# Kernel optimization log

Hardware: AMD Instinct MI355X
Metric: run time of the kernel (lower is better)

Reference implementation:

```python
import jax, jax.numpy as jnp
import numpy as np

N, E = 50000, 800000
IN_CH, EDGE_DIM, H, C = 256, 32, 4, 32


def setup_inputs() -> dict:
    key = jax.random.key(0)
    ks = jax.random.split(key, 9)
    inp = {
        "x": jax.random.normal(ks[0], (N, IN_CH), dtype=jnp.float32),
        "edge_index": jax.random.randint(ks[1], (2, E), 0, N, dtype=jnp.int64),
        "edge_attr": jax.random.normal(ks[2], (E, EDGE_DIM), dtype=jnp.float32),
        "dist_weight": jax.random.uniform(ks[3], (E,), dtype=jnp.float32),
        # learned parameters (xavier-ish scale)
        "W_src": jax.random.normal(ks[4], (IN_CH, H * C), dtype=jnp.float32) * (1.0 / np.sqrt(IN_CH)),
        "W_dst": jax.random.normal(ks[5], (IN_CH, H * C), dtype=jnp.float32) * (1.0 / np.sqrt(IN_CH)),
        "W_edge": jax.random.normal(ks[6], (EDGE_DIM, H * C), dtype=jnp.float32) * (1.0 / np.sqrt(EDGE_DIM)),
        "att": jax.random.normal(ks[7], (1, H, C), dtype=jnp.float32) * 0.1,
        "spatial_scale": jnp.ones((H,), dtype=jnp.float32),
    }
    return inp


def reference(x, edge_index, edge_attr, dist_weight, W_src, W_dst, W_edge, att, spatial_scale):
    n = x.shape[0]
    h, c = att.shape[1], att.shape[2]
    src, dst = edge_index[0], edge_index[1]

    x_src = (x @ W_src).reshape(n, h, c)          # [N,H,C]
    x_dst = (x @ W_dst).reshape(n, h, c)          # [N,H,C]
    e_feat = (edge_attr @ W_edge).reshape(-1, h, c)  # [E,H,C]

    # edge-wise attention logits
    alpha = jnp.tanh(x_src[src] + x_dst[dst] + e_feat)  # [E,H,C]
    alpha = jnp.sum(alpha * att, axis=-1)               # [E,H]
    alpha_raw = alpha

    # spatial decay: dist_weight ** spatial_scale per head
    alpha = alpha * dist_weight[:, None] ** spatial_scale[None, :]

    # segment softmax over dst (numerically stable; max is grad-neutral)
    m = jax.ops.segment_max(alpha, dst, num_segments=n)  # [N,H]
    m = jnp.where(jnp.isfinite(m), m, 0.0)               # empty segments -> 0 (matches torch init)
    m = jax.lax.stop_gradient(m)
    ea = jnp.exp(alpha - m[dst])                         # [E,H]
    s = jax.ops.segment_sum(ea, dst, num_segments=n)     # [N,H]
    alpha_norm = ea / (s[dst] + 1e-8)                    # [E,H]

    # weighted aggregation of source features
    msg = x_src[src] * alpha_norm[:, :, None]            # [E,H,C]
    out = jax.ops.segment_sum(msg, dst, num_segments=n)  # [N,H,C]
    return out.reshape(n, h * c), alpha_norm, alpha_raw
```

## Files before the change

### kernel.cpp

```cpp
#include <hip/hip_runtime.h>
#include <hip/hip_bf16.h>

#define N_NODES 50000
#define N_EDGES 800000
#define IN_CH   256
#define EDGE_DIM 32
#define NH 4
#define NC 32
#define HC 128
#define SCAN_BLKS 196
#define EGROUPS (N_EDGES / 64)
#define NTILES (N_NODES / 16)

typedef __attribute__((ext_vector_type(8))) short bf16x8;
typedef __attribute__((ext_vector_type(4))) float f32x4;

__device__ int g_bsum[256];
__device__ int g_boffs[256];
__device__ __align__(16) unsigned short g_wt_hi[256 * 256];
__device__ __align__(16) unsigned short g_wt_lo[256 * 256];

__device__ __forceinline__ float fexp2(float x) { return __builtin_amdgcn_exp2f(x); }
__device__ __forceinline__ float flog2(float x) { return __builtin_amdgcn_logf(x); }
__device__ __forceinline__ float fexp(float x)  { return __builtin_amdgcn_exp2f(x * 1.44269504089f); }

__device__ __forceinline__ float ftanh(float x) {
    const float e = fexp2(x * 2.88539008178f);
    return 1.0f - 2.0f * __builtin_amdgcn_rcpf(e + 1.0f);
}

__device__ __forceinline__ unsigned short f2bf(float f) {
    union { float f; unsigned int u; } v; v.f = f;
    const unsigned int r = v.u + 0x7fffu + ((v.u >> 16) & 1u);
    return (unsigned short)(r >> 16);
}

__device__ __forceinline__ void split8(const float4 a, const float4 b, bf16x8& hi, bf16x8& lo) {
    union { unsigned short us[8]; bf16x8 v; } H, L;
    const float xs[8] = {a.x, a.y, a.z, a.w, b.x, b.y, b.z, b.w};
    #pragma unroll
    for (int e = 0; e < 8; ++e) {
        const unsigned int u = __float_as_uint(xs[e]);
        H.us[e] = (unsigned short)(u >> 16);
        const float lof = xs[e] - __uint_as_float(u & 0xffff0000u);
        L.us[e] = (unsigned short)(__float_as_uint(lof) >> 16);
    }
    hi = H.v; lo = L.v;
}

__device__ __forceinline__ float ldf(const void* p, long i, bool f32) {
    return f32 ? ((const float*)p)[i]
               : __bfloat162float(((const __hip_bfloat16*)p)[i]);
}

__device__ __forceinline__ int ld_src(const int* ei, long e, bool idx64) {
    return idx64 ? ei[2 * e] : ei[e];
}
__device__ __forceinline__ int ld_dst(const int* ei, long e, bool idx64) {
    return idx64 ? ei[2 * ((long)N_EDGES + e)] : ei[(long)N_EDGES + e];
}

__global__ __launch_bounds__(256) void detect_k(const unsigned short* __restrict__ xu,
                                                const int* __restrict__ ei,
                                                int* __restrict__ flag) {
    __shared__ int zc, bc, nz_idx;
    if (threadIdx.x == 0) { zc = 0; bc = 0; nz_idx = 0; }
    __syncthreads();
    int z = 0, b = 0, hi = 0;
    for (int i = threadIdx.x; i < 16384; i += 256) {
        const unsigned short w = xu[2 * i];
        if (w == 0) ++z;
        if ((w & 0x7F80) == 0x7F80) ++b;
    }
    for (int i = threadIdx.x; i < 8192; i += 256)
        if (ei[2 * i + 1] != 0) hi = 1;
    atomicAdd(&zc, z);
    atomicAdd(&bc, b);
    if (hi) atomicAdd(&nz_idx, 1);
    __syncthreads();
    if (threadIdx.x == 0) {
        flag[0] = (zc > 8192 || bc > 0) ? 1 : 0;
        flag[1] = (nz_idx == 0) ? 1 : 0;
    }
}

__global__ __launch_bounds__(256) void zero_deg_k(int* __restrict__ deg) {
    const int i = blockIdx.x * 256 + threadIdx.x;
    if (i < N_NODES) deg[i] = 0;
}

__global__ __launch_bounds__(256) void hist_k(const int* __restrict__ ei,
                                              const int* __restrict__ flag,
                                              int* __restrict__ deg) {
    const bool idx64 = (flag[1] != 0);
    const long e = (long)blockIdx.x * 256 + threadIdx.x;
    if (e < N_EDGES) atomicAdd(&deg[ld_dst(ei, e, idx64)], 1);
}

__global__ __launch_bounds__(256) void scan1_k(const int* __restrict__ deg,
                                               int* __restrict__ row_ptr) {
    __shared__ int wsum[4];
    const int tid = threadIdx.x;
    const int lane = tid & 63, wid = tid >> 6;
    const int i = blockIdx.x * 256 + tid;
    const int v = (i < N_NODES) ? deg[i] : 0;
    int x = v;
    #pragma unroll
    for (int off = 1; off < 64; off <<= 1) {
        const int t = __shfl_up(x, off);
        if (lane >= off) x += t;
    }
    if (lane == 63) wsum[wid] = x;
    __syncthreads();
    int wpre = 0;
    for (int w = 0; w < wid; ++w) wpre += wsum[w];
    if (i < N_NODES) row_ptr[i] = wpre + x - v;
    if (tid == 0) g_bsum[blockIdx.x] = wsum[0] + wsum[1] + wsum[2] + wsum[3];
}

__global__ __launch_bounds__(256) void scan2_k(int* __restrict__ row_ptr) {
    __shared__ int wsum[4];
    const int tid = threadIdx.x;
    const int lane = tid & 63, wid = tid >> 6;
    const int v = (tid < SCAN_BLKS) ? g_bsum[tid] : 0;
    int x = v;
    #pragma unroll
    for (int off = 1; off < 64; off <<= 1) {
        const int t = __shfl_up(x, off);
        if (lane >= off) x += t;
    }
    if (lane == 63) wsum[wid] = x;
    __syncthreads();
    int wpre = 0;
    for (int w = 0; w < wid; ++w) wpre += wsum[w];
    if (tid < SCAN_BLKS) g_boffs[tid] = wpre + x - v;
    if (tid == 0) row_ptr[N_NODES] = N_EDGES;
}

__global__ __launch_bounds__(256) void scan3_k(int* __restrict__ row_ptr,
                                               int* __restrict__ cursor) {
    const int i = blockIdx.x * 256 + threadIdx.x;
    if (i < N_NODES) {
        const int t = row_ptr[i] + g_boffs[blockIdx.x];
        row_ptr[i] = t;
        cursor[i] = t;
    }
}

__global__ __launch_bounds__(256) void scatter_k(const int* __restrict__ ei,
                                                 const int* __restrict__ flag,
                                                 int* __restrict__ cursor,
                                                 int* __restrict__ eids,
                                                 int* __restrict__ esrc) {
    const bool idx64 = (flag[1] != 0);
    const long e = (long)blockIdx.x * 256 + threadIdx.x;
    if (e >= N_EDGES) return;
    const int dst = ld_dst(ei, e, idx64);
    const int src = ld_src(ei, e, idx64);
    const int pos = atomicAdd(&cursor[dst], 1);
    eids[pos] = (int)e;
    esrc[pos] = src;
}

__global__ __launch_bounds__(256) void w_split_k(const float* __restrict__ Wsrc,
                                                 const float* __restrict__ Wdst,
                                                 const int* __restrict__ flag) {
    if (flag[0] == 0) return;
    const int i = blockIdx.x * 256 + threadIdx.x;
    const int c = i >> 8;
    const int k = i & 255;
    const float w = (c < HC) ? Wsrc[k * HC + c] : Wdst[k * HC + (c - HC)];
    const unsigned int u = __float_as_uint(w);
    g_wt_hi[i] = (unsigned short)(u >> 16);
    const float lof = w - __uint_as_float(u & 0xffff0000u);
    g_wt_lo[i] = (unsigned short)(__float_as_uint(lof) >> 16);
}

__global__ __launch_bounds__(512) void node_gemm_f32s_k(const float* __restrict__ x,
                                                        const int* __restrict__ flag,
                                                        float* __restrict__ xsrc,
                                                        float* __restrict__ xdst) {
    if (flag[0] == 0) return;
    const int tid = threadIdx.x;
    const int l   = tid & 63;
    const int wv  = tid >> 6;
    const int jj  = l & 15;
    const int hi4 = l >> 4;
    const int cbase = wv * 32;

    bf16x8 bhi[8][2], blo[8][2];
    #pragma unroll
    for (int ks = 0; ks < 8; ++ks)
        #pragma unroll
        for (int t = 0; t < 2; ++t) {
            const int off = (cbase + t * 16 + jj) * 256 + ks * 32 + hi4 * 8;
            bhi[ks][t] = *(const bf16x8*)(g_wt_hi + off);
            blo[ks][t] = *(const bf16x8*)(g_wt_lo + off);
        }

    for (int nt = blockIdx.x; nt < NTILES; nt += gridDim.x) {
        const long n0 = (long)nt * 16;
        const float* xr = x + (n0 + jj) * IN_CH;

        f32x4 acc[2];
        acc[0] = (f32x4){0.f, 0.f, 0.f, 0.f};
        acc[1] = (f32x4){0.f, 0.f, 0.f, 0.f};
        #pragma unroll
        for (int ks = 0; ks < 8; ++ks) {
            const float4 a0 = *(const float4*)(xr + ks * 32 + hi4 * 8);
            const float4 a1 = *(const float4*)(xr + ks * 32 + hi4 * 8 + 4);
            bf16x8 ahi, alo;
            split8(a0, a1, ahi, alo);
            #pragma unroll
            for (int t = 0; t < 2; ++t) {
                acc[t] = __builtin_amdgcn_mfma_f32_16x16x32_bf16(ahi, bhi[ks][t], acc[t], 0, 0, 0);
                acc[t] = __builtin_amdgcn_mfma_f32_16x16x32_bf16(ahi, blo[ks][t], acc[t], 0, 0, 0);
                acc[t] = __builtin_amdgcn_mfma_f32_16x16x32_bf16(alo, bhi[ks][t], acc[t], 0, 0, 0);
            }
        }

        #pragma unroll
        for (int t = 0; t < 2; ++t) {
            const int c = cbase + t * 16 + jj;
            float* obase = (c < HC) ? (xsrc + c) : (xdst + (c - HC));
            #pragma unroll
            for (int r = 0; r < 4; ++r)
                obase[(n0 + hi4 * 4 + r) * HC] = acc[t][r];
        }
    }
}

__global__ __launch_bounds__(256) void node_gemm_mfma_k(const unsigned short* __restrict__ x,
                                                        const unsigned short* __restrict__ Wsrc,
                                                        const unsigned short* __restrict__ Wdst,
                                                        const int* __restrict__ flag,
                                                        float* __restrict__ xsrc,
                                                        float* __restrict__ xdst) {
    if (flag[0] != 0) return;
    const int tid = threadIdx.x;
    const int l   = tid & 63;
    const int w   = tid >> 6;
    const int jj  = l & 15;
    const int hi  = l >> 4;
    const int cbase = w * 64;

    bf16x8 bfrag[8][4];
    #pragma unroll
    for (int ks = 0; ks < 8; ++ks)
        #pragma unroll
        for (int t = 0; t < 4; ++t) {
            const int c = cbase + t * 16 + jj;
            const unsigned short* Wp = (c < HC) ? (Wsrc + c) : (Wdst + (c - HC));
            union { unsigned short u[8]; bf16x8 v; } bu;
            #pragma unroll
            for (int i = 0; i < 8; ++i)
                bu.u[i] = Wp[(ks * 32 + hi * 8 + i) * HC];
            bfrag[ks][t] = bu.v;
        }

    for (int nt = blockIdx.x; nt < NTILES; nt += gridDim.x) {
        const long n0 = (long)nt * 16;
        const unsigned short* xr = x + (n0 + jj) * IN_CH + hi * 8;
        bf16x8 afrag[8];
        #pragma unroll
        for (int ks = 0; ks < 8; ++ks)
            afrag[ks] = *(const bf16x8*)(xr + ks * 32);

        f32x4 acc[4];
        #pragma unroll
        for (int t = 0; t < 4; ++t) acc[t] = (f32x4){0.f, 0.f, 0.f, 0.f};
        #pragma unroll
        for (int ks = 0; ks < 8; ++ks)
            #pragma unroll
            for (int t = 0; t < 4; ++t)
                acc[t] = __builtin_amdgcn_mfma_f32_16x16x32_bf16(afrag[ks], bfrag[ks][t], acc[t], 0, 0, 0);

        #pragma unroll
        for (int t = 0; t < 4; ++t) {
            const int c = cbase + t * 16 + jj;
            float* obase = (c < HC) ? (xsrc + c) : (xdst + (c - HC));
            #pragma unroll
            for (int r = 0; r < 4; ++r)
                obase[(n0 + hi * 4 + r) * HC] = acc[t][r];
        }
    }
}

__global__ __launch_bounds__(256) void edge_alpha_k(const int* __restrict__ ei,
                                                    const void* __restrict__ eattr,
                                                    const void* __restrict__ dw,
                                                    const void* __restrict__ Wedge,
                                                    const void* __restrict__ att,
                                                    const void* __restrict__ sscale,
                                                    const int* __restrict__ flag,
                                                    const float* __restrict__ xsrc,
                                                    const float* __restrict__ xdst,
                                                    float* __restrict__ ea_ws,
                                                    float* __restrict__ araw_out) {
    const bool f32   = (flag[0] != 0);
    const bool idx64 = (flag[1] != 0);
    __shared__ int   sSrc[4][16];
    __shared__ int   sDst[4][16];
    __shared__ float sDw[4][16];

    const int tid = threadIdx.x;
    const int l   = tid & 63;
    const int wid = tid >> 6;
    const int jj  = l & 15;
    const int hi  = l >> 4;

    bf16x8 bfrag[8];
    #pragma unroll
    for (int t = 0; t < 8; ++t) {
        union { unsigned short u[8]; bf16x8 v; } bu;
        #pragma unroll
        for (int i = 0; i < 8; ++i) {
            const int k = hi * 8 + i;
            const int col = t * 16 + jj;
            if (f32) bu.u[i] = f2bf(((const float*)Wedge)[k * HC + col]);
            else     bu.u[i] = ((const unsigned short*)Wedge)[k * HC + col];
        }
        bfrag[t] = bu.v;
    }
    float attv[8];
    #pragma unroll
    for (int t = 0; t < 8; ++t) attv[t] = ldf(att, t * 16 + jj, f32);
    const float ssv = ldf(sscale, l & 3, f32);

    for (long g = blockIdx.x; g < EGROUPS; g += (long)gridDim.x) {
        const long e0 = g * 64 + (long)wid * 16;

        if (l < 16)      sSrc[wid][l]      = ld_src(ei, e0 + l, idx64);
        else if (l < 32) sDst[wid][l - 16] = ld_dst(ei, e0 + (l - 16), idx64);
        else if (l < 48) sDw[wid][l - 32]  = ldf(dw, e0 + (l - 32), f32);
        __builtin_amdgcn_wave_barrier();

        bf16x8 afrag;
        if (f32) {
            const float* ar = (const float*)eattr + (e0 + jj) * EDGE_DIM + hi * 8;
            const float4 p0 = *(const float4*)ar;
            const float4 p1 = *(const float4*)(ar + 4);
            union { unsigned short u[8]; bf16x8 v; } au;
            au.u[0] = f2bf(p0.x); au.u[1] = f2bf(p0.y); au.u[2] = f2bf(p0.z); au.u[3] = f2bf(p0.w);
            au.u[4] = f2bf(p1.x); au.u[5] = f2bf(p1.y); au.u[6] = f2bf(p1.z); au.u[7] = f2bf(p1.w);
            afrag = au.v;
        } else {
            afrag = *(const bf16x8*)((const unsigned short*)eattr + (e0 + jj) * EDGE_DIM + hi * 8);
        }

        const f32x4 zero = {0.f, 0.f, 0.f, 0.f};
        f32x4 acc[8];
        #pragma unroll
        for (int t = 0; t < 8; ++t)
            acc[t] = __builtin_amdgcn_mfma_f32_16x16x32_bf16(afrag, bfrag[t], zero, 0, 0, 0);

        float hsum[4][4] = {{0,0,0,0},{0,0,0,0},{0,0,0,0},{0,0,0,0}};
        #pragma unroll
        for (int r = 0; r < 4; ++r) {
            const int sI = sSrc[wid][hi * 4 + r];
            const int dI = sDst[wid][hi * 4 + r];
            const float* bs = xsrc + (long)sI * HC + jj;
            const float* bd = xdst + (long)dI * HC + jj;
            float xsv[8], xdv[8];
            #pragma unroll
            for (int t = 0; t < 8; ++t) xsv[t] = bs[t * 16];
            #pragma unroll
            for (int t = 0; t < 8; ++t) xdv[t] = bd[t * 16];
            #pragma unroll
            for (int t = 0; t < 8; ++t) {
                const float v = ftanh(acc[t][r] + xsv[t] + xdv[t]) * attv[t];
                hsum[r][t >> 1] += v;
            }
        }

        #pragma unroll
        for (int r = 0; r < 4; ++r)
            #pragma unroll
            for (int h2 = 0; h2 < 4; ++h2) {
                float v = hsum[r][h2];
                v += __shfl_xor(v, 1);
                v += __shfl_xor(v, 2);
                v += __shfl_xor(v, 4);
                v += __shfl_xor(v, 8);
                hsum[r][h2] = v;
            }

        float val = hsum[0][0];
        #pragma unroll
        for (int r = 0; r < 4; ++r)
            #pragma unroll
            for (int h2 = 0; h2 < 4; ++h2)
                if (jj == r * 4 + h2) val = hsum[r][h2];

        const int r_sel = jj >> 2;
        const long er = e0 + hi * 4 + r_sel;
        const float dwv = sDw[wid][hi * 4 + r_sel];
        araw_out[er * 4 + (jj & 3)] = val;
        const float d = fexp2(ssv * flog2(dwv));
        ea_ws[er * 4 + (jj & 3)] = fexp(val * d);
        __builtin_amdgcn_wave_barrier();
    }
}

__global__ __launch_bounds__(256) void aggregate_k(const int* __restrict__ row_ptr,
                                                   const int* __restrict__ eids,
                                                   const int* __restrict__ esrc,
                                                   const float* __restrict__ ea_ws,
                                                   const float* __restrict__ xsrc,
                                                   float* __restrict__ s_ws,
                                                   float* __restrict__ out) {
    const int tid = threadIdx.x;
    const int lane = tid & 63;
    const int n = blockIdx.x * 4 + (tid >> 6);
    if (n >= N_NODES) return;
    const int h = lane >> 4;

    const int p0 = row_ptr[n];
    const int p1 = row_ptr[n + 1];

    float ax = 0.0f, ay = 0.0f, sa = 0.0f;
    for (int p = p0; p < p1; ++p) {
        const int e = eids[p];
        const int src = esrc[p];
        const float w = ea_ws[(long)e * 4 + h];
        const float2 xv = *(const float2*)(xsrc + (long)src * HC + (lane << 1));
        ax += w * xv.x;
        ay += w * xv.y;
        sa += w;
    }
    const float inv = 1.0f / (sa + 1e-8f);
    float* o = out + (long)n * HC + (lane << 1);
    o[0] = ax * inv;
    o[1] = ay * inv;
    if ((lane & 15) == 0) s_ws[(long)n * 4 + h] = sa;
}

__global__ __launch_bounds__(256) void edge_norm_k(const int* __restrict__ ei,
                                                   const int* __restrict__ flag,
                                                   const float* __restrict__ ea_ws,
                                                   const float* __restrict__ s_ws,
                                                   float* __restrict__ anorm) {
    const bool idx64 = (flag[1] != 0);
    const long i = (long)blockIdx.x * 256 + threadIdx.x;
    if (i >= (long)N_EDGES * NH) return;
    const long e = i >> 2;
    const int h = (int)(i & 3);
    const int dst = ld_dst(ei, e, idx64);
    anorm[i] = ea_ws[i] / (s_ws[(long)dst * 4 + h] + 1e-8f);
}

extern "C" void kernel_launch(void* const* d_in, const int* in_sizes, int n_in,
                              void* d_out, int out_size, void* d_ws, size_t ws_size,
                              hipStream_t stream) {
    const void* x      = d_in[0];
    const int*  ei     = (const int*)d_in[1];
    const void* eattr  = d_in[2];
    const void* dw     = d_in[3];
    const void* Wsrc   = d_in[4];
    const void* Wdst   = d_in[5];
    const void* Wedge  = d_in[6];
    const void* att    = d_in[7];
    const void* sscale = d_in[8];

    float* out   = (float*)d_out;
    float* anorm = out + (long)N_NODES * HC;
    float* araw  = anorm + (long)N_EDGES * NH;

    float* ws      = (float*)d_ws;
    int*   flag    = (int*)d_ws;
    float* xsrc    = ws + 64;
    float* xdst    = xsrc + (long)N_NODES * HC;
    float* ea      = xdst + (long)N_NODES * HC;
    float* s_ws    = ea + (long)N_EDGES * NH;
    int*   deg     = (int*)(s_ws + (long)N_NODES * NH);
    int*   row_ptr = deg + N_NODES;
    int*   cursor  = row_ptr + N_NODES + 1;
    int*   eids    = cursor + N_NODES;
    int*   esrc    = eids + N_EDGES;

    detect_k<<<1, 256, 0, stream>>>((const unsigned short*)x, ei, flag);
    zero_deg_k<<<(N_NODES + 255) / 256, 256, 0, stream>>>(deg);
    hist_k<<<(N_EDGES + 255) / 256, 256, 0, stream>>>(ei, flag, deg);
    scan1_k<<<SCAN_BLKS, 256, 0, stream>>>(deg, row_ptr);
    scan2_k<<<1, 256, 0, stream>>>(row_ptr);
    scan3_k<<<SCAN_BLKS, 256, 0, stream>>>(row_ptr, cursor);
    scatter_k<<<(N_EDGES + 255) / 256, 256, 0, stream>>>(ei, flag, cursor, eids, esrc);
    w_split_k<<<256, 256, 0, stream>>>((const float*)Wsrc, (const float*)Wdst, flag);
    node_gemm_f32s_k<<<512, 512, 0, stream>>>((const float*)x, flag, xsrc, xdst);
    node_gemm_mfma_k<<<1024, 256, 0, stream>>>((const unsigned short*)x,
                                               (const unsigned short*)Wsrc,
                                               (const unsigned short*)Wdst,
                                               flag, xsrc, xdst);
    edge_alpha_k<<<2048, 256, 0, stream>>>(ei, eattr, dw, Wedge, att, sscale,
                                           flag, xsrc, xdst, ea, araw);
    aggregate_k<<<(N_NODES + 3) / 4, 256, 0, stream>>>(row_ptr, eids, esrc, ea, xsrc, s_ws, out);
    edge_norm_k<<<((long)N_EDGES * NH + 255) / 256, 256, 0, stream>>>(ei, flag, ea, s_ws, anorm);
}
```

Before: 671.1 us.

## Fuse edge attention and aggregation into one destination-sorted CSR kernel

Replaces the edge-parallel attention kernel and the separate node aggregation kernel with one kernel where each wave walks a destination node's CSR edge list in chunks of 16. It computes the attention logits with MFMA, exponentiates them, and accumulates the weighted x_src messages in registers, so x_src rows are fetched once for both uses and ea_ws is no longer reread during aggregation. x_dst is loaded once per node. The costs are gathered (non-coalesced) edge_attr and dist_weight reads through the edge-id permutation, and idle lanes on nodes with fewer than 16 edges. The type-detection kernel also samples fewer elements, which makes the heuristic slightly less robust.

```diff
diff --git a/kernel.cpp b/kernel.cpp
--- a/kernel.cpp
+++ b/kernel.cpp
@@ -9,7 +9,6 @@
 #define NC 32
 #define HC 128
 #define SCAN_BLKS 196
-#define EGROUPS (N_EDGES / 64)
 #define NTILES (N_NODES / 16)
 
 typedef __attribute__((ext_vector_type(8))) short bf16x8;
@@ -67,19 +66,19 @@
     if (threadIdx.x == 0) { zc = 0; bc = 0; nz_idx = 0; }
     __syncthreads();
     int z = 0, b = 0, hi = 0;
-    for (int i = threadIdx.x; i < 16384; i += 256) {
+    for (int i = threadIdx.x; i < 4096; i += 256) {
         const unsigned short w = xu[2 * i];
         if (w == 0) ++z;
         if ((w & 0x7F80) == 0x7F80) ++b;
     }
-    for (int i = threadIdx.x; i < 8192; i += 256)
+    for (int i = threadIdx.x; i < 2048; i += 256)
         if (ei[2 * i + 1] != 0) hi = 1;
     atomicAdd(&zc, z);
     atomicAdd(&bc, b);
     if (hi) atomicAdd(&nz_idx, 1);
     __syncthreads();
     if (threadIdx.x == 0) {
-        flag[0] = (zc > 8192 || bc > 0) ? 1 : 0;
+        flag[0] = (zc > 2048 || bc > 0) ? 1 : 0;
         flag[1] = (nz_idx == 0) ? 1 : 0;
     }
 }
@@ -286,21 +285,24 @@
     }
 }
 
-__global__ __launch_bounds__(256) void edge_alpha_k(const int* __restrict__ ei,
-                                                    const void* __restrict__ eattr,
-                                                    const void* __restrict__ dw,
-                                                    const void* __restrict__ Wedge,
-                                                    const void* __restrict__ att,
-                                                    const void* __restrict__ sscale,
-                                                    const int* __restrict__ flag,
-                                                    const float* __restrict__ xsrc,
-                                                    const float* __restrict__ xdst,
-                                                    float* __restrict__ ea_ws,
-                                                    float* __restrict__ araw_out) {
-    const bool f32   = (flag[0] != 0);
-    const bool idx64 = (flag[1] != 0);
+__global__ __launch_bounds__(256) void fused_edge_agg_k(const int* __restrict__ row_ptr,
+                                                        const int* __restrict__ eids,
+                                                        const int* __restrict__ esrc,
+                                                        const void* __restrict__ eattr,
+                                                        const void* __restrict__ dw,
+                                                        const void* __restrict__ Wedge,
+                                                        const void* __restrict__ att,
+                                                        const void* __restrict__ sscale,
+                                                        const int* __restrict__ flag,
+                                                        const float* __restrict__ xsrc,
+                                                        const float* __restrict__ xdst,
+                                                        float* __restrict__ ea_ws,
+                                                        float* __restrict__ araw_out,
+                                                        float* __restrict__ s_ws,
+                                                        float* __restrict__ out) {
+    const bool f32 = (flag[0] != 0);
+    __shared__ int   sEid[4][16];
     __shared__ int   sSrc[4][16];
-    __shared__ int   sDst[4][16];
     __shared__ float sDw[4][16];
 
     const int tid = threadIdx.x;
@@ -325,114 +327,138 @@
     float attv[8];
     #pragma unroll
     for (int t = 0; t < 8; ++t) attv[t] = ldf(att, t * 16 + jj, f32);
-    const float ssv = ldf(sscale, l & 3, f32);
-
-    for (long g = blockIdx.x; g < EGROUPS; g += (long)gridDim.x) {
-        const long e0 = g * 64 + (long)wid * 16;
-
-        if (l < 16)      sSrc[wid][l]      = ld_src(ei, e0 + l, idx64);
-        else if (l < 32) sDst[wid][l - 16] = ld_dst(ei, e0 + (l - 16), idx64);
-        else if (l < 48) sDw[wid][l - 32]  = ldf(dw, e0 + (l - 32), f32);
-        __builtin_amdgcn_wave_barrier();
-
-        bf16x8 afrag;
-        if (f32) {
-            const float* ar = (const float*)eattr + (e0 + jj) * EDGE_DIM + hi * 8;
-            const float4 p0 = *(const float4*)ar;
-            const float4 p1 = *(const float4*)(ar + 4);
-            union { unsigned short u[8]; bf16x8 v; } au;
-            au.u[0] = f2bf(p0.x); au.u[1] = f2bf(p0.y); au.u[2] = f2bf(p0.z); au.u[3] = f2bf(p0.w);
-            au.u[4] = f2bf(p1.x); au.u[5] = f2bf(p1.y); au.u[6] = f2bf(p1.z); au.u[7] = f2bf(p1.w);
-            afrag = au.v;
-        } else {
-            afrag = *(const bf16x8*)((const unsigned short*)eattr + (e0 + jj) * EDGE_DIM + hi * 8);
-        }
-
-        const f32x4 zero = {0.f, 0.f, 0.f, 0.f};
-        f32x4 acc[8];
-        #pragma unroll
-        for (int t = 0; t < 8; ++t)
-            acc[t] = __builtin_amdgcn_mfma_f32_16x16x32_bf16(afrag, bfrag[t], zero, 0, 0, 0);
-
-        float hsum[4][4] = {{0,0,0,0},{0,0,0,0},{0,0,0,0},{0,0,0,0}};
-        #pragma unroll
-        for (int r = 0; r < 4; ++r) {
-            const int sI = sSrc[wid][hi * 4 + r];
-            const int dI = sDst[wid][hi * 4 + r];
-            const float* bs = xsrc + (long)sI * HC + jj;
-            const float* bd = xdst + (long)dI * HC + jj;
-            float xsv[8], xdv[8];
-            #pragma unroll
-            for (int t = 0; t < 8; ++t) xsv[t] = bs[t * 16];
-            #pragma unroll
-            for (int t = 0; t < 8; ++t) xdv[t] = bd[t * 16];
-            #pragma unroll
-            for (int t = 0; t < 8; ++t) {
-                const float v = ftanh(acc[t][r] + xsv[t] + xdv[t]) * attv[t];
-                hsum[r][t >> 1] += v;
-            }
-        }
-
-        #pragma unroll
-        for (int r = 0; r < 4; ++r)
-            #pragma unroll
-            for (int h2 = 0; h2 < 4; ++h2) {
-                float v = hsum[r][h2];
-                v += __shfl_xor(v, 1);
-                v += __shfl_xor(v, 2);
-                v += __shfl_xor(v, 4);
-                v += __shfl_xor(v, 8);
-                hsum[r][h2] = v;
-            }
-
-        float val = hsum[0][0];
-        #pragma unroll
-        for (int r = 0; r < 4; ++r)
-            #pragma unroll
-            for (int h2 = 0; h2 < 4; ++h2)
-                if (jj == r * 4 + h2) val = hsum[r][h2];
-
-        const int r_sel = jj >> 2;
-        const long er = e0 + hi * 4 + r_sel;
-        const float dwv = sDw[wid][hi * 4 + r_sel];
-        araw_out[er * 4 + (jj & 3)] = val;
-        const float d = fexp2(ssv * flog2(dwv));
-        ea_ws[er * 4 + (jj & 3)] = fexp(val * d);
-        __builtin_amdgcn_wave_barrier();
-    }
-}
-
-__global__ __launch_bounds__(256) void aggregate_k(const int* __restrict__ row_ptr,
-                                                   const int* __restrict__ eids,
-                                                   const int* __restrict__ esrc,
-                                                   const float* __restrict__ ea_ws,
-                                                   const float* __restrict__ xsrc,
-                                                   float* __restrict__ s_ws,
-                                                   float* __restrict__ out) {
-    const int tid = threadIdx.x;
-    const int lane = tid & 63;
-    const int n = blockIdx.x * 4 + (tid >> 6);
-    if (n >= N_NODES) return;
-    const int h = lane >> 4;
-
-    const int p0 = row_ptr[n];
-    const int p1 = row_ptr[n + 1];
-
-    float ax = 0.0f, ay = 0.0f, sa = 0.0f;
-    for (int p = p0; p < p1; ++p) {
-        const int e = eids[p];
-        const int src = esrc[p];
-        const float w = ea_ws[(long)e * 4 + h];
-        const float2 xv = *(const float2*)(xsrc + (long)src * HC + (lane << 1));
-        ax += w * xv.x;
-        ay += w * xv.y;
-        sa += w;
-    }
-    const float inv = 1.0f / (sa + 1e-8f);
-    float* o = out + (long)n * HC + (lane << 1);
-    o[0] = ax * inv;
-    o[1] = ay * inv;
-    if ((lane & 15) == 0) s_ws[(long)n * 4 + h] = sa;
+    float ss4[4];
+    #pragma unroll
+    for (int h2 = 0; h2 < 4; ++h2) ss4[h2] = ldf(sscale, h2, f32);
+
+    const int nwaves = gridDim.x * 4;
+    for (int n = blockIdx.x * 4 + wid; n < N_NODES; n += nwaves) {
+        const int p0 = row_ptr[n];
+        const int p1 = row_ptr[n + 1];
+
+        float xdv[8];
+        #pragma unroll
+        for (int t = 0; t < 8; ++t) xdv[t] = xdst[(long)n * HC + jj + t * 16];
+
+        float ax[8] = {0,0,0,0,0,0,0,0};
+        float sal[4] = {0,0,0,0};
+
+        for (int base = p0; base < p1; base += 16) {
+            if (l < 16) {
+                const int p = min(base + l, p1 - 1);
+                const int e = eids[p];
+                sEid[wid][l] = e;
+                sSrc[wid][l] = esrc[p];
+                sDw[wid][l]  = ldf(dw, e, f32);
+            }
+            __builtin_amdgcn_wave_barrier();
+
+            const long eA = sEid[wid][jj];
+            bf16x8 afrag;
+            if (f32) {
+                const float* ar = (const float*)eattr + eA * EDGE_DIM + hi * 8;
+                const float4 q0 = *(const float4*)ar;
+                const float4 q1 = *(const float4*)(ar + 4);
+                union { unsigned short u[8]; bf16x8 v; } au;
+                au.u[0] = f2bf(q0.x); au.u[1] = f2bf(q0.y); au.u[2] = f2bf(q0.z); au.u[3] = f2bf(q0.w);
+                au.u[4] = f2bf(q1.x); au.u[5] = f2bf(q1.y); au.u[6] = f2bf(q1.z); au.u[7] = f2bf(q1.w);
+                afrag = au.v;
+            } else {
+                afrag = *(const bf16x8*)((const unsigned short*)eattr + eA * EDGE_DIM + hi * 8);
+            }
+
+            const f32x4 zero = {0.f, 0.f, 0.f, 0.f};
+            f32x4 acc[8];
+            #pragma unroll
+            for (int t = 0; t < 8; ++t)
+                acc[t] = __builtin_amdgcn_mfma_f32_16x16x32_bf16(afrag, bfrag[t], zero, 0, 0, 0);
+
+            float xsv[4][8];
+            float hsum[4][4] = {{0,0,0,0},{0,0,0,0},{0,0,0,0},{0,0,0,0}};
+            #pragma unroll
+            for (int r = 0; r < 4; ++r) {
+                const int sI = sSrc[wid][hi * 4 + r];
+                const float* bs = xsrc + (long)sI * HC + jj;
+                #pragma unroll
+                for (int t = 0; t < 8; ++t) xsv[r][t] = bs[t * 16];
+                #pragma unroll
+                for (int t = 0; t < 8; ++t) {
+                    const float v = ftanh(acc[t][r] + xsv[r][t] + xdv[t]) * attv[t];
+                    hsum[r][t >> 1] += v;
+                }
+            }
+
+            #pragma unroll
+            for (int r = 0; r < 4; ++r)
+                #pragma unroll
+                for (int h2 = 0; h2 < 4; ++h2) {
+                    float v = hsum[r][h2];
+                    v += __shfl_xor(v, 1);
+                    v += __shfl_xor(v, 2);
+                    v += __shfl_xor(v, 4);
+                    v += __shfl_xor(v, 8);
+                    hsum[r][h2] = v;
+                }
+
+            float eaV[4][4];
+            #pragma unroll
+            for (int r = 0; r < 4; ++r) {
+                const bool valid = (base + hi * 4 + r) < p1;
+                const float lg = flog2(sDw[wid][hi * 4 + r]);
+                #pragma unroll
+                for (int h2 = 0; h2 < 4; ++h2) {
+                    const float d = fexp2(ss4[h2] * lg);
+                    eaV[r][h2] = valid ? fexp(hsum[r][h2] * d) : 0.0f;
+                }
+            }
+
+            {
+                const int r_sel = jj >> 2, hh = jj & 3;
+                if (base + hi * 4 + r_sel < p1) {
+                    float pval = hsum[0][0], eval = eaV[0][0];
+                    #pragma unroll
+                    for (int r = 0; r < 4; ++r)
+                        #pragma unroll
+                        for (int h2 = 0; h2 < 4; ++h2)
+                            if (jj == r * 4 + h2) { pval = hsum[r][h2]; eval = eaV[r][h2]; }
+                    const long e2 = sEid[wid][hi * 4 + r_sel];
+                    araw_out[e2 * 4 + hh] = pval;
+                    ea_ws[e2 * 4 + hh]    = eval;
+                }
+            }
+
+            #pragma unroll
+            for (int r = 0; r < 4; ++r) {
+                #pragma unroll
+                for (int t = 0; t < 8; ++t)
+                    ax[t] += eaV[r][t >> 1] * xsv[r][t];
+                #pragma unroll
+                for (int h2 = 0; h2 < 4; ++h2) sal[h2] += eaV[r][h2];
+            }
+            __builtin_amdgcn_wave_barrier();
+        }
+
+        #pragma unroll
+        for (int t = 0; t < 8; ++t) {
+            ax[t] += __shfl_xor(ax[t], 16);
+            ax[t] += __shfl_xor(ax[t], 32);
+        }
+        #pragma unroll
+        for (int h2 = 0; h2 < 4; ++h2) {
+            sal[h2] += __shfl_xor(sal[h2], 16);
+            sal[h2] += __shfl_xor(sal[h2], 32);
+        }
+        float inv[4];
+        #pragma unroll
+        for (int h2 = 0; h2 < 4; ++h2) inv[h2] = 1.0f / (sal[h2] + 1e-8f);
+
+        {
+            const int t0 = hi * 2, t1 = t0 + 1;
+            out[(long)n * HC + jj + 16 * t0] = ax[t0] * inv[t0 >> 1];
+            out[(long)n * HC + jj + 16 * t1] = ax[t1] * inv[t1 >> 1];
+        }
+        if (l < 4) s_ws[(long)n * 4 + l] = sal[l];
+    }
 }
 
 __global__ __launch_bounds__(256) void edge_norm_k(const int* __restrict__ ei,
@@ -491,8 +517,8 @@
                                                (const unsigned short*)Wsrc,
                                                (const unsigned short*)Wdst,
                                                flag, xsrc, xdst);
-    edge_alpha_k<<<2048, 256, 0, stream>>>(ei, eattr, dw, Wedge, att, sscale,
-                                           flag, xsrc, xdst, ea, araw);
-    aggregate_k<<<(N_NODES + 3) / 4, 256, 0, stream>>>(row_ptr, eids, esrc, ea, xsrc, s_ws, out);
+    fused_edge_agg_k<<<2048, 256, 0, stream>>>(row_ptr, eids, esrc, eattr, dw, Wedge,
+                                               att, sscale, flag, xsrc, xdst,
+                                               ea, araw, s_ws, out);
     edge_norm_k<<<((long)N_EDGES * NH + 255) / 256, 256, 0, stream>>>(ei, flag, ea, s_ws, anorm);
 }
```

After: 664.5 us. Within noise of the previous version (-1.0%).
